# Optimization experiments

Hardware: AMD Instinct MI355X
Metric: run time of the kernel (lower is better)

The kernel has to match this reference:

```python
import jax, jax.numpy as jnp
import numpy as np

N_NODES = 50000
N_EDGES = 800000
D_NODE = 64
D_EDGE = 64
D_OUT = 64
D_HID = 128
LN_EPS = 1e-5


def _mlp_params(key, d_in):
    # layer sizes: [d_in, D_HID, D_HID, D_OUT]; weights stored [in, out]
    ks = jax.random.split(key, 3)
    dims = [d_in, D_HID, D_HID, D_OUT]
    params = []
    for i in range(3):
        s = 1.0 / np.sqrt(dims[i])
        params.append(jax.random.uniform(ks[i], (dims[i], dims[i + 1]), minval=-s, maxval=s, dtype=jnp.float32))
        params.append(jnp.zeros((dims[i + 1],), jnp.float32))
    # LayerNorm gamma/beta
    params.append(jnp.ones((D_OUT,), jnp.float32))
    params.append(jnp.zeros((D_OUT,), jnp.float32))
    return params


def _mlp_ln(h, W0, b0, W1, b1, W2, b2, g, beta):
    h = jax.nn.relu(h @ W0 + b0)
    h = jax.nn.relu(h @ W1 + b1)
    h = h @ W2 + b2
    mu = jnp.mean(h, axis=-1, keepdims=True)
    var = jnp.mean(jnp.square(h - mu), axis=-1, keepdims=True)
    return (h - mu) * jax.lax.rsqrt(var + LN_EPS) * g + beta


def setup_inputs() -> dict:
    key = jax.random.key(0)
    k = jax.random.split(key, 8)
    inp = {
        "x": jax.random.normal(k[0], (N_NODES, D_NODE), jnp.float32),
        "mesh_edge_index": jax.random.randint(k[1], (2, N_EDGES), 0, N_NODES, dtype=jnp.int32),
        "mesh_edge_attr": jax.random.normal(k[2], (N_EDGES, D_EDGE), jnp.float32),
        "world_edge_index": jax.random.randint(k[3], (2, N_EDGES), 0, N_NODES, dtype=jnp.int32),
        "world_edge_attr": jax.random.normal(k[4], (N_EDGES, D_EDGE), jnp.float32),
    }
    names = ["W0", "b0", "W1", "b1", "W2", "b2", "ln_g", "ln_b"]
    for pref, kk, d_in in [("mesh", k[5], 2 * D_NODE + D_EDGE),
                           ("world", k[6], 2 * D_NODE + D_EDGE),
                           ("upd", k[7], D_NODE + 2 * D_OUT)]:
        ps = _mlp_params(kk, d_in)
        for nm, p in zip(names, ps):
            inp[f"{pref}_{nm}"] = p
    return inp


def _edge_block(x, edge_index, edge_attr, W0, b0, W1, b1, W2, b2, g, beta):
    src, dst = edge_index[0], edge_index[1]  # PyG: x_j = source, x_i = target
    x_i = x[dst]  # [E, D_NODE]
    x_j = x[src]
    concat = jnp.concatenate([x_i, x_j, edge_attr], axis=-1)  # [E, 2D+De]
    new_edge = edge_attr + _mlp_ln(concat, W0, b0, W1, b1, W2, b2, g, beta)
    agg = jax.ops.segment_sum(new_edge, dst, num_segments=N_NODES)  # 'add' aggr at target
    return agg, new_edge


def reference(x, mesh_edge_index, mesh_edge_attr, world_edge_index, world_edge_attr,
              mesh_W0, mesh_b0, mesh_W1, mesh_b1, mesh_W2, mesh_b2, mesh_ln_g, mesh_ln_b,
              world_W0, world_b0, world_W1, world_b1, world_W2, world_b2, world_ln_g, world_ln_b,
              upd_W0, upd_b0, upd_W1, upd_b1, upd_W2, upd_b2, upd_ln_g, upd_ln_b):
    agg_m, new_edge_m = _edge_block(x, mesh_edge_index, mesh_edge_attr,
                                    mesh_W0, mesh_b0, mesh_W1, mesh_b1, mesh_W2, mesh_b2, mesh_ln_g, mesh_ln_b)
    agg_w, new_edge_w = _edge_block(x, world_edge_index, world_edge_attr,
                                    world_W0, world_b0, world_W1, world_b1, world_W2, world_b2, world_ln_g, world_ln_b)
    concat = jnp.concatenate([x, agg_m, agg_w], axis=-1)  # [N, D_NODE + 2*D_OUT]
    x_new = x + _mlp_ln(concat, upd_W0, upd_b0, upd_W1, upd_b1, upd_W2, upd_b2, upd_ln_g, upd_ln_b)
    return x_new, new_edge_m, new_edge_w
```

## Files before the change

### kernel.cpp

```cpp
#include <hip/hip_runtime.h>


#define NNODES 50000
#define NEDGES 800000
#define NBLK 512

typedef __bf16 bf16x8 __attribute__((ext_vector_type(8)));
typedef float f32x4 __attribute__((ext_vector_type(4)));
#define MFMA(a, b, c) __builtin_amdgcn_mfma_f32_16x16x32_bf16(a, b, c, 0, 0, 0)

#define OFF_A 0
#define OFF_H0 24576
#define OFF_P 40960
#define OFF_PAR 43008
#define SMEM 44800

__device__ __forceinline__ unsigned short f2bf(float f) {
  unsigned u = __builtin_bit_cast(unsigned, f);
  u = (u + 0x7fffu + ((u >> 16) & 1u)) >> 16;
  return (unsigned short)u;
}
__device__ __forceinline__ unsigned long long pk4(f32x4 v) {
  union { unsigned short h[4]; unsigned long long u; } p;
  p.h[0] = f2bf(v[0]); p.h[1] = f2bf(v[1]); p.h[2] = f2bf(v[2]); p.h[3] = f2bf(v[3]);
  return p.u;
}
__device__ __forceinline__ int4 pk8(float4 a, float4 b) {
  union { unsigned short us[8]; int4 v; } u;
  u.us[0] = f2bf(a.x); u.us[1] = f2bf(a.y); u.us[2] = f2bf(a.z); u.us[3] = f2bf(a.w);
  u.us[4] = f2bf(b.x); u.us[5] = f2bf(b.y); u.us[6] = f2bf(b.z); u.us[7] = f2bf(b.w);
  return u.v;
}
__device__ __forceinline__ int4 ldpk(const float* p) {
  return pk8(*(const float4*)p, *(const float4*)(p + 4));
}

template <bool EDGE>
__global__ __launch_bounds__(512, 4) void mlp_block(
    const float* __restrict__ g1, const float* __restrict__ g2,
    const float* __restrict__ g3, const int* __restrict__ srcI,
    const int* __restrict__ dstI, const unsigned short* __restrict__ Wt,
    const float* __restrict__ b0, const float* __restrict__ b1,
    const float* __restrict__ b2, const float* __restrict__ gam,
    const float* __restrict__ bet, float* __restrict__ outp, int M) {
  __shared__ __align__(16) char sm[SMEM];
  const int tid = threadIdx.x, lane = tid & 63, wave = tid >> 6;
  const int lrow = lane & 15, cg = lane >> 4;
  const unsigned short* Wt0 = Wt;
  const unsigned short* Wt1 = Wt + 24576;
  const unsigned short* Wt2 = Wt + 40960;
  const int ntiles = (M + 63) >> 6;
  const int cg2 = wave & 3, rg = wave >> 2;

  for (int i = tid; i < 448; i += 512) {
    float v;
    if (i < 128) v = b0[i];
    else if (i < 256) v = b1[i - 128];
    else if (i < 320) v = b2[i - 256];
    else if (i < 384) v = gam[i - 320];
    else v = bet[i - 384];
    ((float*)(sm + OFF_PAR))[i] = v;
  }
  const float* PAR = (const float*)(sm + OFF_PAR);

  bf16x8 w0f[6], w1f[4], w2f[4];
#pragma unroll
  for (int kk = 0; kk < 6; ++kk)
    w0f[kk] = *(const bf16x8*)(Wt0 + (wave * 16 + lrow) * 192 + kk * 32 + cg * 8);
#pragma unroll
  for (int kk = 0; kk < 4; ++kk)
    w1f[kk] = *(const bf16x8*)(Wt1 + (wave * 16 + lrow) * 128 + kk * 32 + cg * 8);
#pragma unroll
  for (int kk = 0; kk < 4; ++kk)
    w2f[kk] = *(const bf16x8*)(Wt2 + (cg2 * 16 + lrow) * 128 + kk * 32 + cg * 8);

  const int srow = (tid >> 5) * 4 + ((tid & 31) >> 3), oct = tid & 7;

  int4 pxd, pxs, pat;
  auto LOADT = [&](int tt) {
    const int row = tt * 64 + srow;
    if (EDGE) {
      const int d = dstI[row], s = srcI[row];
      pxd = ldpk(g1 + (size_t)d * 64 + oct * 8);
      pxs = ldpk(g1 + (size_t)s * 64 + oct * 8);
      pat = ldpk(g3 + (size_t)row * 64 + oct * 8);
    } else {
      const int rr = min(row, M - 1);
      pxd = ldpk(g1 + (size_t)rr * 64 + oct * 8);
      pxs = ldpk(g2 + (size_t)rr * 64 + oct * 8);
      pat = ldpk(g3 + (size_t)rr * 64 + oct * 8);
    }
  };
  auto STAGE = [&]() {
    char* a0 = sm + OFF_A + srow * 384;
    const int swz = (srow & 7) << 4;
    *(int4*)(a0 + ((oct * 16) ^ swz)) = pxd;
    *(int4*)(a0 + ((128 + oct * 16) ^ swz)) = pxs;
    *(int4*)(a0 + ((256 + oct * 16) ^ swz)) = pat;
  };

  int t = blockIdx.x;
  if (t >= ntiles) return;
  LOADT(t);
  STAGE();

  for (; t < ntiles; t += NBLK) {
    const int tn = t + NBLK;
    const bool more = tn < ntiles;
    __syncthreads();
    if (more) LOADT(tn);
    {
      const f32x4 bb0 = *(const f32x4*)(PAR + wave * 16 + cg * 4);
#pragma unroll
      for (int rt = 0; rt < 4; ++rt) {
        const int row = rt * 16 + lrow, swz = (row & 7) << 4;
        const char* ab = sm + OFF_A + row * 384;
        f32x4 acc = {0.f, 0.f, 0.f, 0.f};
#pragma unroll
        for (int kk = 0; kk < 6; ++kk)
          acc = MFMA(w0f[kk], *(const bf16x8*)(ab + ((kk * 64 + cg * 16) ^ swz)), acc);
        f32x4 h;
#pragma unroll
        for (int q = 0; q < 4; ++q) h[q] = fmaxf(acc[q] + bb0[q], 0.f);
        *(unsigned long long*)(sm + OFF_H0 + row * 256 + ((wave * 32 + cg * 8) ^ swz)) = pk4(h);
      }
    }
    __syncthreads();
    {
      const f32x4 bb1 = *(const f32x4*)(PAR + 128 + wave * 16 + cg * 4);
#pragma unroll
      for (int rt = 0; rt < 4; ++rt) {
        const int row = rt * 16 + lrow, swz = (row & 7) << 4;
        const char* hb = sm + OFF_H0 + row * 256;
        f32x4 acc = {0.f, 0.f, 0.f, 0.f};
#pragma unroll
        for (int kk = 0; kk < 4; ++kk)
          acc = MFMA(w1f[kk], *(const bf16x8*)(hb + ((kk * 64 + cg * 16) ^ swz)), acc);
        f32x4 h;
#pragma unroll
        for (int q = 0; q < 4; ++q) h[q] = fmaxf(acc[q] + bb1[q], 0.f);
        *(unsigned long long*)(sm + OFF_A + row * 384 + ((wave * 32 + cg * 8) ^ swz)) = pk4(h);
      }
    }
    __syncthreads();
    f32x4 accE[2];
    {
      const f32x4 bb2 = *(const f32x4*)(PAR + 256 + cg2 * 16 + cg * 4);
#pragma unroll
      for (int j = 0; j < 2; ++j) {
        const int row = (rg * 2 + j) * 16 + lrow, swz = (row & 7) << 4;
        const char* hb = sm + OFF_A + row * 384;
        f32x4 acc = {0.f, 0.f, 0.f, 0.f};
#pragma unroll
        for (int kk = 0; kk < 4; ++kk)
          acc = MFMA(w2f[kk], *(const bf16x8*)(hb + ((kk * 64 + cg * 16) ^ swz)), acc);
#pragma unroll
        for (int q = 0; q < 4; ++q) acc[q] += bb2[q];
        float s = acc[0] + acc[1] + acc[2] + acc[3];
        float ss = acc[0] * acc[0] + acc[1] * acc[1] + acc[2] * acc[2] + acc[3] * acc[3];
        s += __shfl_xor(s, 16, 64); s += __shfl_xor(s, 32, 64);
        ss += __shfl_xor(ss, 16, 64); ss += __shfl_xor(ss, 32, 64);
        if (cg == 0) *(float2*)(sm + OFF_P + row * 32 + cg2 * 8) = make_float2(s, ss);
        accE[j] = acc;
      }
    }
    __syncthreads();
    {
      const f32x4 gv = *(const f32x4*)(PAR + 320 + cg2 * 16 + cg * 4);
      const f32x4 bv = *(const f32x4*)(PAR + 384 + cg2 * 16 + cg * 4);
#pragma unroll
      for (int j = 0; j < 2; ++j) {
        const int row = (rg * 2 + j) * 16 + lrow, gr = t * 64 + row;
        float4 p0 = *(const float4*)(sm + OFF_P + row * 32);
        float4 p1 = *(const float4*)(sm + OFF_P + row * 32 + 16);
        float s = p0.x + p0.z + p1.x + p1.z, ss = p0.y + p0.w + p1.y + p1.w;
        float mean = s * (1.f / 64.f);
        float var = fmaxf(ss * (1.f / 64.f) - mean * mean, 0.f);
        float inv = rsqrtf(var + 1e-5f);
        const int col = cg2 * 16 + cg * 4;
        const int grc = EDGE ? gr : min(gr, M - 1);
        const f32x4 r = *(const f32x4*)(g3 + (size_t)grc * 64 + col);
        f32x4 a = accE[j], o;
#pragma unroll
        for (int q = 0; q < 4; ++q) o[q] = (a[q] - mean) * inv * gv[q] + bv[q] + r[q];
        if (EDGE || gr < M) *(f32x4*)(outp + (size_t)gr * 64 + col) = o;
      }
    }
    if (more) STAGE();
  }
}

__global__ __launch_bounds__(256) void agg_k(const float* __restrict__ oute,
                                             const int* __restrict__ perm,
                                             const int* __restrict__ rp,
                                             float* __restrict__ agg) {
  const int lane = threadIdx.x & 63;
  const int r4 = lane >> 4, cq = lane & 15;
  const int w = (blockIdx.x * 256 + threadIdx.x) >> 6;
  const int nw = gridDim.x * 4;
  for (int d = w; d < NNODES; d += nw) {
    const int s = rp[d], e = rp[d + 1];
    f32x4 acc = {0.f, 0.f, 0.f, 0.f};
    for (int j = s + r4; j < e; j += 4) {
      const int row = perm[j];
      const f32x4 v = *(const f32x4*)(oute + (size_t)row * 64 + cq * 4);
#pragma unroll
      for (int q = 0; q < 4; ++q) acc[q] += v[q];
    }
#pragma unroll
    for (int q = 0; q < 4; ++q) {
      acc[q] += __shfl_xor(acc[q], 16, 64);
      acc[q] += __shfl_xor(acc[q], 32, 64);
    }
    if (r4 == 0) *(f32x4*)(agg + (size_t)d * 64 + cq * 4) = acc;
  }
}

struct PrepArgs { const float* w[9]; unsigned short* wt[3]; };

__global__ void prep_w(PrepArgs pa) {
  int i = blockIdx.x * 256 + threadIdx.x;
  if (i >= 3 * 49152) return;
  int mlp = i / 49152;
  int rem = i - mlp * 49152;
  int mat, off, K, N;
  if (rem < 24576)      { mat = 0; off = 0;     K = 192; N = 128; }
  else if (rem < 40960) { mat = 1; off = 24576; K = 128; N = 128; }
  else                  { mat = 2; off = 40960; K = 128; N = 64;  }
  int local = rem - off;
  int n = local / K, k = local - n * K;
  if (mlp == 2 && mat == 0) k = (k + 64) % 192;
  pa.wt[mlp][rem] = f2bf(pa.w[mlp * 3 + mat][k * N + n]);
}

__global__ void zero_f4(float4* p, int n) {
  int i = blockIdx.x * blockDim.x + threadIdx.x;
  if (i < n) p[i] = make_float4(0.f, 0.f, 0.f, 0.f);
}

__global__ void hist_k(const int* __restrict__ dM, const int* __restrict__ dW,
                       int* __restrict__ curM, int* __restrict__ curW, int E) {
  int i = blockIdx.x * 256 + threadIdx.x;
  if (i < E) {
    atomicAdd(curM + dM[i], 1);
    atomicAdd(curW + dW[i], 1);
  }
}

__global__ __launch_bounds__(1024) void scan_k(int* __restrict__ curM, int* __restrict__ curW,
                                               int* __restrict__ rpM, int* __restrict__ rpW) {
  __shared__ int buf[1024];
  int* cur = blockIdx.x ? curW : curM;
  int* rp = blockIdx.x ? rpW : rpM;
  const int tid = threadIdx.x, base = tid * 49;
  const int lim = min(base + 49, NNODES);
  int p = 0;
  for (int b = base; b < lim; ++b) p += cur[b];
  buf[tid] = p;
  __syncthreads();
  const int own = p;
  for (int off = 1; off < 1024; off <<= 1) {
    int nv = (tid >= off) ? buf[tid - off] : 0;
    __syncthreads();
    buf[tid] += nv;
    __syncthreads();
  }
  int running = buf[tid] - own;
  for (int b = base; b < lim; ++b) {
    int h = cur[b];
    cur[b] = running;
    rp[b] = running;
    running += h;
  }
  if (tid == 1023) rp[NNODES] = buf[1023];
}

__global__ void scatter_k(const int* __restrict__ dM, const int* __restrict__ dW,
                          int* __restrict__ curM, int* __restrict__ curW,
                          int* __restrict__ permM, int* __restrict__ permW, int E) {
  int i = blockIdx.x * 256 + threadIdx.x;
  if (i < E) {
    int p = atomicAdd(curM + dM[i], 1);
    permM[p] = i;
    p = atomicAdd(curW + dW[i], 1);
    permW[p] = i;
  }
}

extern "C" void kernel_launch(void* const* d_in, const int* in_sizes, int n_in,
                              void* d_out, int out_size, void* d_ws, size_t ws_size,
                              hipStream_t stream) {
  const float* x      = (const float*)d_in[0];
  const int*   meIdx  = (const int*)d_in[1];
  const float* meAttr = (const float*)d_in[2];
  const int*   weIdx  = (const int*)d_in[3];
  const float* weAttr = (const float*)d_in[4];

  float* out_x  = (float*)d_out;
  float* out_em = out_x + (size_t)NNODES * 64;
  float* out_ew = out_em + (size_t)NEDGES * 64;

  char* ws = (char*)d_ws;
  unsigned short* WtM = (unsigned short*)ws;
  unsigned short* WtW = (unsigned short*)(ws + 98304);
  unsigned short* WtU = (unsigned short*)(ws + 196608);
  float* aggm = (float*)(ws + 294912);
  float* aggw = aggm + (size_t)NNODES * 64;
  char* p = ws + 294912 + 25600000;
  int* curM  = (int*)p;
  int* curW  = curM + NNODES;
  int* rpM   = (int*)(p + 400000);
  int* rpW   = rpM + 50016;
  int* permM = rpW + 50016;
  int* permW = permM + NEDGES;

  zero_f4<<<dim3(98), dim3(256), 0, stream>>>((float4*)curM, 25000);

  PrepArgs pa;
  for (int m = 0; m < 3; ++m)
    for (int l = 0; l < 3; ++l)
      pa.w[m * 3 + l] = (const float*)d_in[5 + m * 8 + l * 2];
  pa.wt[0] = WtM; pa.wt[1] = WtW; pa.wt[2] = WtU;
  prep_w<<<dim3(576), dim3(256), 0, stream>>>(pa);

  hist_k<<<dim3(3125), dim3(256), 0, stream>>>(meIdx + NEDGES, weIdx + NEDGES, curM, curW, NEDGES);
  scan_k<<<dim3(2), dim3(1024), 0, stream>>>(curM, curW, rpM, rpW);
  scatter_k<<<dim3(3125), dim3(256), 0, stream>>>(meIdx + NEDGES, weIdx + NEDGES,
                                                  curM, curW, permM, permW, NEDGES);

  mlp_block<true><<<dim3(NBLK), dim3(512), 0, stream>>>(
      x, x, meAttr, meIdx, meIdx + NEDGES, WtM,
      (const float*)d_in[6], (const float*)d_in[8], (const float*)d_in[10],
      (const float*)d_in[11], (const float*)d_in[12],
      out_em, NEDGES);
  mlp_block<true><<<dim3(NBLK), dim3(512), 0, stream>>>(
      x, x, weAttr, weIdx, weIdx + NEDGES, WtW,
      (const float*)d_in[14], (const float*)d_in[16], (const float*)d_in[18],
      (const float*)d_in[19], (const float*)d_in[20],
      out_ew, NEDGES);

  agg_k<<<dim3(1024), dim3(256), 0, stream>>>(out_em, permM, rpM, aggm);
  agg_k<<<dim3(1024), dim3(256), 0, stream>>>(out_ew, permW, rpW, aggw);

  mlp_block<false><<<dim3(NBLK), dim3(512), 0, stream>>>(
      aggm, aggw, x, nullptr, nullptr, WtU,
      (const float*)d_in[22], (const float*)d_in[24], (const float*)d_in[26],
      (const float*)d_in[27], (const float*)d_in[28],
      out_x, NNODES);
}
```

Before: 931.5 us.

## Pre-convert node features to bf16, parallelize CSR scan, merge and unroll aggregation

Node features are converted to bf16 once up front, so the edge MLP gathers half as many bytes per endpoint and skips per-edge conversion. The single-block-per-set serial prefix scan is replaced by a three-stage chunked scan that spreads across many blocks. The two aggregation launches are merged into one larger grid, and the gather loop is unrolled by two with independent accumulators to raise memory-level parallelism. These changes add a kernel launch for the conversion and two for the scan, and use extra workspace.

```diff
diff --git a/kernel.cpp b/kernel.cpp
--- a/kernel.cpp
+++ b/kernel.cpp
@@ -4,6 +4,7 @@
 #define NNODES 50000
 #define NEDGES 800000
 #define NBLK 512
+#define NCHUNK 196
 
 typedef __bf16 bf16x8 __attribute__((ext_vector_type(8)));
 typedef float f32x4 __attribute__((ext_vector_type(4)));
@@ -38,8 +39,9 @@
 template <bool EDGE>
 __global__ __launch_bounds__(512, 4) void mlp_block(
     const float* __restrict__ g1, const float* __restrict__ g2,
-    const float* __restrict__ g3, const int* __restrict__ srcI,
-    const int* __restrict__ dstI, const unsigned short* __restrict__ Wt,
+    const float* __restrict__ g3, const unsigned short* __restrict__ xb,
+    const int* __restrict__ srcI, const int* __restrict__ dstI,
+    const unsigned short* __restrict__ Wt,
     const float* __restrict__ b0, const float* __restrict__ b1,
     const float* __restrict__ b2, const float* __restrict__ gam,
     const float* __restrict__ bet, float* __restrict__ outp, int M) {
@@ -80,9 +82,9 @@
   auto LOADT = [&](int tt) {
     const int row = tt * 64 + srow;
     if (EDGE) {
-      const int d = dstI[row], s = srcI[row];
-      pxd = ldpk(g1 + (size_t)d * 64 + oct * 8);
-      pxs = ldpk(g1 + (size_t)s * 64 + oct * 8);
+      const int d = dstI[row], s2 = srcI[row];
+      pxd = *(const int4*)(xb + (size_t)d * 64 + oct * 8);
+      pxs = *(const int4*)(xb + (size_t)s2 * 64 + oct * 8);
       pat = ldpk(g3 + (size_t)row * 64 + oct * 8);
     } else {
       const int rr = min(row, M - 1);
@@ -180,9 +182,9 @@
         const int col = cg2 * 16 + cg * 4;
         const int grc = EDGE ? gr : min(gr, M - 1);
         const f32x4 r = *(const f32x4*)(g3 + (size_t)grc * 64 + col);
-        f32x4 a = accE[j], o;
-#pragma unroll
-        for (int q = 0; q < 4; ++q) o[q] = (a[q] - mean) * inv * gv[q] + bv[q] + r[q];
+        f32x4 av = accE[j], o;
+#pragma unroll
+        for (int q = 0; q < 4; ++q) o[q] = (av[q] - mean) * inv * gv[q] + bv[q] + r[q];
         if (EDGE || gr < M) *(f32x4*)(outp + (size_t)gr * 64 + col) = o;
       }
     }
@@ -190,28 +192,47 @@
   }
 }
 
-__global__ __launch_bounds__(256) void agg_k(const float* __restrict__ oute,
-                                             const int* __restrict__ perm,
-                                             const int* __restrict__ rp,
-                                             float* __restrict__ agg) {
+__global__ __launch_bounds__(256) void agg_k(const float* __restrict__ em,
+                                             const float* __restrict__ ew,
+                                             const int* __restrict__ permM,
+                                             const int* __restrict__ permW,
+                                             const int* __restrict__ rpM,
+                                             const int* __restrict__ rpW,
+                                             float* __restrict__ aggm,
+                                             float* __restrict__ aggw) {
   const int lane = threadIdx.x & 63;
   const int r4 = lane >> 4, cq = lane & 15;
   const int w = (blockIdx.x * 256 + threadIdx.x) >> 6;
   const int nw = gridDim.x * 4;
-  for (int d = w; d < NNODES; d += nw) {
+  for (int dd = w; dd < 2 * NNODES; dd += nw) {
+    const bool s1 = dd >= NNODES;
+    const int d = s1 ? dd - NNODES : dd;
+    const float* oute = s1 ? ew : em;
+    const int* perm = s1 ? permW : permM;
+    const int* rp = s1 ? rpW : rpM;
     const int s = rp[d], e = rp[d + 1];
-    f32x4 acc = {0.f, 0.f, 0.f, 0.f};
-    for (int j = s + r4; j < e; j += 4) {
-      const int row = perm[j];
-      const f32x4 v = *(const f32x4*)(oute + (size_t)row * 64 + cq * 4);
-#pragma unroll
-      for (int q = 0; q < 4; ++q) acc[q] += v[q];
+    f32x4 acc = {0.f, 0.f, 0.f, 0.f}, acc2 = {0.f, 0.f, 0.f, 0.f};
+    int j = s + r4;
+    for (; j + 4 < e; j += 8) {
+      const int ra = perm[j], rb = perm[j + 4];
+      const f32x4 va = *(const f32x4*)(oute + (size_t)ra * 64 + cq * 4);
+      const f32x4 vb = *(const f32x4*)(oute + (size_t)rb * 64 + cq * 4);
+#pragma unroll
+      for (int q = 0; q < 4; ++q) { acc[q] += va[q]; acc2[q] += vb[q]; }
+    }
+    if (j < e) {
+      const int ra = perm[j];
+      const f32x4 va = *(const f32x4*)(oute + (size_t)ra * 64 + cq * 4);
+#pragma unroll
+      for (int q = 0; q < 4; ++q) acc[q] += va[q];
     }
 #pragma unroll
     for (int q = 0; q < 4; ++q) {
+      acc[q] += acc2[q];
       acc[q] += __shfl_xor(acc[q], 16, 64);
       acc[q] += __shfl_xor(acc[q], 32, 64);
     }
+    float* agg = s1 ? aggw : aggm;
     if (r4 == 0) *(f32x4*)(agg + (size_t)d * 64 + cq * 4) = acc;
   }
 }
@@ -233,6 +254,11 @@
   pa.wt[mlp][rem] = f2bf(pa.w[mlp * 3 + mat][k * N + n]);
 }
 
+__global__ void prep_x(const float* __restrict__ x, unsigned short* __restrict__ xb) {
+  int i = blockIdx.x * 256 + threadIdx.x;
+  if (i < NNODES * 8) *(int4*)(xb + (size_t)i * 8) = ldpk(x + (size_t)i * 8);
+}
+
 __global__ void zero_f4(float4* p, int n) {
   int i = blockIdx.x * blockDim.x + threadIdx.x;
   if (i < n) p[i] = make_float4(0.f, 0.f, 0.f, 0.f);
@@ -247,32 +273,73 @@
   }
 }
 
-__global__ __launch_bounds__(1024) void scan_k(int* __restrict__ curM, int* __restrict__ curW,
-                                               int* __restrict__ rpM, int* __restrict__ rpW) {
-  __shared__ int buf[1024];
-  int* cur = blockIdx.x ? curW : curM;
-  int* rp = blockIdx.x ? rpW : rpM;
-  const int tid = threadIdx.x, base = tid * 49;
-  const int lim = min(base + 49, NNODES);
-  int p = 0;
-  for (int b = base; b < lim; ++b) p += cur[b];
-  buf[tid] = p;
+__global__ __launch_bounds__(64) void csum_k(const int* __restrict__ curM,
+                                             const int* __restrict__ curW,
+                                             int* __restrict__ csum) {
+  const int c = blockIdx.x, set = c >= NCHUNK, c0 = c - set * NCHUNK;
+  const int* cnt = set ? curW : curM;
+  const int lane = threadIdx.x;
+  const int base = c0 * 256 + lane * 4;
+  int s = 0;
+  if (base + 3 < NNODES) {
+    int4 v = *(const int4*)(cnt + base);
+    s = v.x + v.y + v.z + v.w;
+  } else {
+    for (int k = 0; k < 4; ++k) if (base + k < NNODES) s += cnt[base + k];
+  }
+#pragma unroll
+  for (int off = 1; off < 64; off <<= 1) s += __shfl_xor(s, off, 64);
+  if (lane == 0) csum[c] = s;
+}
+
+__global__ __launch_bounds__(512) void cscan_k(const int* __restrict__ csum,
+                                               int* __restrict__ cbase) {
+  __shared__ int buf[512];
+  const int tid = threadIdx.x;
+  buf[tid] = (tid < 2 * NCHUNK) ? csum[tid] : 0;
   __syncthreads();
-  const int own = p;
-  for (int off = 1; off < 1024; off <<= 1) {
+  for (int off = 1; off < 512; off <<= 1) {
     int nv = (tid >= off) ? buf[tid - off] : 0;
     __syncthreads();
     buf[tid] += nv;
     __syncthreads();
   }
-  int running = buf[tid] - own;
-  for (int b = base; b < lim; ++b) {
-    int h = cur[b];
-    cur[b] = running;
-    rp[b] = running;
-    running += h;
-  }
-  if (tid == 1023) rp[NNODES] = buf[1023];
+  if (tid < 2 * NCHUNK) {
+    const int set = tid >= NCHUNK;
+    int excl = tid ? buf[tid - 1] : 0;
+    if (set) excl -= buf[NCHUNK - 1];
+    cbase[tid] = excl;
+  }
+}
+
+__global__ __launch_bounds__(64) void rp_k(int* __restrict__ curM, int* __restrict__ curW,
+                                           const int* __restrict__ cbase,
+                                           int* __restrict__ rpM, int* __restrict__ rpW) {
+  const int c = blockIdx.x, set = c >= NCHUNK, c0 = c - set * NCHUNK;
+  int* cnt = set ? curW : curM;
+  int* rp = set ? rpW : rpM;
+  const int lane = threadIdx.x;
+  const int idx = c0 * 256 + lane * 4;
+  int v[4];
+#pragma unroll
+  for (int k = 0; k < 4; ++k) v[k] = (idx + k < NNODES) ? cnt[idx + k] : 0;
+  const int ls = v[0] + v[1] + v[2] + v[3];
+  int ex = ls;
+#pragma unroll
+  for (int off = 1; off < 64; off <<= 1) {
+    int nv = __shfl_up(ex, off, 64);
+    if (lane >= off) ex += nv;
+  }
+  int run = cbase[c] + (ex - ls);
+#pragma unroll
+  for (int k = 0; k < 4; ++k) {
+    if (idx + k < NNODES) {
+      rp[idx + k] = run;
+      cnt[idx + k] = run;
+      run += v[k];
+    }
+  }
+  if (c0 == 0 && lane == 0) rp[NNODES] = NEDGES;
 }
 
 __global__ void scatter_k(const int* __restrict__ dM, const int* __restrict__ dW,
@@ -304,15 +371,18 @@
   unsigned short* WtM = (unsigned short*)ws;
   unsigned short* WtW = (unsigned short*)(ws + 98304);
   unsigned short* WtU = (unsigned short*)(ws + 196608);
-  float* aggm = (float*)(ws + 294912);
-  float* aggw = aggm + (size_t)NNODES * 64;
-  char* p = ws + 294912 + 25600000;
+  unsigned short* xb  = (unsigned short*)(ws + 294912);
+  float* aggm = (float*)(ws + 6694912);
+  float* aggw = (float*)(ws + 19494912);
+  char* p = ws + 32294912;
   int* curM  = (int*)p;
   int* curW  = curM + NNODES;
   int* rpM   = (int*)(p + 400000);
   int* rpW   = rpM + 50016;
   int* permM = rpW + 50016;
   int* permW = permM + NEDGES;
+  int* csum  = permW + NEDGES;
+  int* cbase = csum + 512;
 
   zero_f4<<<dim3(98), dim3(256), 0, stream>>>((float4*)curM, 25000);
 
@@ -322,28 +392,30 @@
       pa.w[m * 3 + l] = (const float*)d_in[5 + m * 8 + l * 2];
   pa.wt[0] = WtM; pa.wt[1] = WtW; pa.wt[2] = WtU;
   prep_w<<<dim3(576), dim3(256), 0, stream>>>(pa);
+  prep_x<<<dim3(1563), dim3(256), 0, stream>>>(x, xb);
 
   hist_k<<<dim3(3125), dim3(256), 0, stream>>>(meIdx + NEDGES, weIdx + NEDGES, curM, curW, NEDGES);
-  scan_k<<<dim3(2), dim3(1024), 0, stream>>>(curM, curW, rpM, rpW);
+  csum_k<<<dim3(2 * NCHUNK), dim3(64), 0, stream>>>(curM, curW, csum);
+  cscan_k<<<dim3(1), dim3(512), 0, stream>>>(csum, cbase);
+  rp_k<<<dim3(2 * NCHUNK), dim3(64), 0, stream>>>(curM, curW, cbase, rpM, rpW);
   scatter_k<<<dim3(3125), dim3(256), 0, stream>>>(meIdx + NEDGES, weIdx + NEDGES,
                                                   curM, curW, permM, permW, NEDGES);
 
   mlp_block<true><<<dim3(NBLK), dim3(512), 0, stream>>>(
-      x, x, meAttr, meIdx, meIdx + NEDGES, WtM,
+      nullptr, nullptr, meAttr, xb, meIdx, meIdx + NEDGES, WtM,
       (const float*)d_in[6], (const float*)d_in[8], (const float*)d_in[10],
       (const float*)d_in[11], (const float*)d_in[12],
       out_em, NEDGES);
   mlp_block<true><<<dim3(NBLK), dim3(512), 0, stream>>>(
-      x, x, weAttr, weIdx, weIdx + NEDGES, WtW,
+      nullptr, nullptr, weAttr, xb, weIdx, weIdx + NEDGES, WtW,
       (const float*)d_in[14], (const float*)d_in[16], (const float*)d_in[18],
       (const float*)d_in[19], (const float*)d_in[20],
       out_ew, NEDGES);
 
-  agg_k<<<dim3(1024), dim3(256), 0, stream>>>(out_em, permM, rpM, aggm);
-  agg_k<<<dim3(1024), dim3(256), 0, stream>>>(out_ew, permW, rpW, aggw);
+  agg_k<<<dim3(4096), dim3(256), 0, stream>>>(out_em, out_ew, permM, permW, rpM, rpW, aggm, aggw);
 
   mlp_block<false><<<dim3(NBLK), dim3(512), 0, stream>>>(
-      aggm, aggw, x, nullptr, nullptr, WtU,
+      aggm, aggw, x, nullptr, nullptr, nullptr, WtU,
       (const float*)d_in[22], (const float*)d_in[24], (const float*)d_in[26],
       (const float*)d_in[27], (const float*)d_in[28],
       out_x, NNODES);
```

Result: faster. 750.3 us (-19.4%).
